# Performance work log

Hardware: AMD Instinct MI355X
Metric: run time of the kernel (lower is better)

## Reference

```python
import jax, jax.numpy as jnp
import numpy as np

NUM_NODES = 100000
NUM_EDGES = 600000
NUM_GRAPHS = 1000
EMB = 128


def setup_inputs() -> dict:
    key = jax.random.key(0)
    ks = jax.random.split(key, 12)
    x = jax.random.normal(ks[0], (NUM_NODES, 4), dtype=jnp.float32)
    edge_index = jax.random.randint(ks[1], (2, NUM_EDGES), 0, NUM_NODES, dtype=jnp.int32)
    x_scalar = jax.random.normal(ks[2], (NUM_GRAPHS, 4), dtype=jnp.float32)
    batch_index = jnp.sort(jax.random.randint(ks[3], (NUM_NODES,), 0, NUM_GRAPHS, dtype=jnp.int32))
    def glorot(k, shape):
        fan_in, fan_out = shape[0], shape[1]
        s = jnp.sqrt(2.0 / (fan_in + fan_out)).astype(jnp.float32)
        return jax.random.normal(k, shape, dtype=jnp.float32) * s
    return {
        "x": x,
        "edge_index": edge_index,
        "x_scalar": x_scalar,
        "batch_index": batch_index,
        "W0": glorot(ks[4], (4, EMB)), "b0": jnp.zeros((EMB,), jnp.float32),
        "W1": glorot(ks[5], (EMB, EMB)), "b1": jnp.zeros((EMB,), jnp.float32),
        "W2": glorot(ks[6], (EMB, EMB)), "b2": jnp.zeros((EMB,), jnp.float32),
        "W3": glorot(ks[7], (EMB, EMB)), "b3": jnp.zeros((EMB,), jnp.float32),
        "Wl1": glorot(ks[8], (EMB + 4, 64)), "bl1": jnp.zeros((64,), jnp.float32),
        "Wl2": glorot(ks[9], (64, 1)), "bl2": jnp.zeros((1,), jnp.float32),
    }


def _gcn_norm(edge_index, num_nodes):
    # PyG GCNConv default: add self-loops, symmetric normalization
    loop = jnp.arange(num_nodes, dtype=edge_index.dtype)
    src = jnp.concatenate([edge_index[0], loop])
    dst = jnp.concatenate([edge_index[1], loop])
    deg = jax.ops.segment_sum(jnp.ones_like(src, dtype=jnp.float32), dst,
                              num_segments=num_nodes)
    dinv = jnp.where(deg > 0, jax.lax.rsqrt(jnp.maximum(deg, 1e-12)), 0.0)
    norm = dinv[src] * dinv[dst]  # [E+N]
    return src, dst, norm


def _gcn_conv(h, src, dst, norm, W, b, num_nodes):
    h = h @ W                                   # [N, out]
    msg = h[src] * norm[:, None]                # gather + normalize
    out = jax.ops.segment_sum(msg, dst, num_segments=num_nodes)  # scatter-add
    return out + b


def reference(x, edge_index, x_scalar, batch_index,
              W0, b0, W1, b1, W2, b2, W3, b3, Wl1, bl1, Wl2, bl2):
    n = x.shape[0]
    src, dst, norm = _gcn_norm(edge_index, n)
    h = jax.nn.relu(_gcn_conv(x, src, dst, norm, W0, b0, n))
    h = jax.nn.relu(_gcn_conv(h, src, dst, norm, W1, b1, n))
    h = jax.nn.relu(_gcn_conv(h, src, dst, norm, W2, b2, n))
    h = jax.nn.relu(_gcn_conv(h, src, dst, norm, W3, b3, n))
    # global mean pool over batch_index
    sums = jax.ops.segment_sum(h, batch_index, num_segments=NUM_GRAPHS)
    cnts = jax.ops.segment_sum(jnp.ones((n,), jnp.float32), batch_index,
                               num_segments=NUM_GRAPHS)
    pooled = sums / jnp.maximum(cnts, 1.0)[:, None]          # [G, EMB]
    feat = jnp.concatenate([pooled, x_scalar], axis=1)       # [G, EMB+4]
    out = jax.nn.relu(feat @ Wl1 + bl1) @ Wl2 + bl2          # [G, 1]
    return out
```

## Files before the change

kernel.cpp:

```cpp
#include <hip/hip_runtime.h>

#define NN 100000
#define EE 600000
#define GG 1000
#define NB ((NN + 255) / 256)
#define CAP 32
#define LDSPAD 136

typedef __bf16 bf16x8 __attribute__((ext_vector_type(8)));
typedef float f32x4 __attribute__((ext_vector_type(4)));
typedef unsigned int u32;

__device__ inline float2 bf2_to_f2(u32 u) {
  return make_float2(__uint_as_float(u << 16), __uint_as_float(u & 0xffff0000u));
}
__device__ inline u32 f2_to_bf2(float a, float b) {
  union { __bf16 h[2]; u32 u; } pk;
  pk.h[0] = (__bf16)a; pk.h[1] = (__bf16)b;
  return pk.u;
}


__global__ void k_init(int* cnt, int* gstart) {
  int i = blockIdx.x * 256 + threadIdx.x;
  if (i < NN) cnt[i] = 0;
  if (i <= GG) gstart[i] = NN;
}

__global__ void k_fill(const int* __restrict__ src, const int* __restrict__ dst,
                       int* cnt, int* __restrict__ ibucket) {
  int e = blockIdx.x * 256 + threadIdx.x;
  if (e >= EE) return;
  int s = src[e], d = dst[e];
  int pos = atomicAdd(&cnt[d], 1);
  if (pos < CAP - 1) ibucket[d * CAP + pos] = s;
}

__global__ void k_prep(const int* __restrict__ cnt, float* __restrict__ dinv,
                       const int* __restrict__ batch, int* gstart,
                       const float* __restrict__ W1, const float* __restrict__ W2,
                       const float* __restrict__ W3,
                       __bf16* __restrict__ Wt1, __bf16* __restrict__ Wt2,
                       __bf16* __restrict__ Wt3) {
  int gid = blockIdx.x * 256 + threadIdx.x;
  if (gid < NN) {
    dinv[gid] = rsqrtf((float)(cnt[gid] + 1));
    int b = batch[gid];
    if (gid == 0) {
      for (int g = 0; g <= b; ++g) gstart[g] = 0;
    } else {
      int prev = batch[gid - 1];
      for (int g = prev + 1; g <= b; ++g) gstart[g] = gid;
    }
  }
  if (gid < 3 * 16384) {
    int which = gid >> 14, idx = gid & 16383;
    int n = idx >> 7, k = idx & 127;
    const float* W = (which == 0) ? W1 : (which == 1) ? W2 : W3;
    __bf16* Wt = (which == 0) ? Wt1 : (which == 1) ? Wt2 : Wt3;
    Wt[(size_t)n * 128 + k] = (__bf16)W[(size_t)k * 128 + n];
  }
}

__global__ void k_wb(const int* __restrict__ ibucket, const int* __restrict__ cnt,
                     const float* __restrict__ dinv, int2* __restrict__ wbucket) {
  int gid = blockIdx.x * 256 + threadIdx.x;
  if (gid >= NN * CAP) return;
  int d = gid >> 5, slot = gid & 31;
  int m = min(cnt[d], CAP - 1);
  int mp = (m + 8) & ~7;
  if (slot >= mp) return;
  float dd = dinv[d];
  int s; float w;
  if (slot < m)      { s = ibucket[gid]; w = dinv[s] * dd; }
  else if (slot == m){ s = d;            w = dd * dd; }
  else               { s = d;            w = 0.f; }
  wbucket[gid] = make_int2(s, __float_as_int(w));
}


__global__ void k_aggx(const float4* __restrict__ x, const int* __restrict__ cnt,
                       const int2* __restrict__ wbucket, float4* __restrict__ y) {
  int i = blockIdx.x * 256 + threadIdx.x;
  if (i >= NN) return;
  int m1 = min(cnt[i], CAP - 1) + 1;
  float4 acc = make_float4(0.f, 0.f, 0.f, 0.f);
  for (int e = 0; e < m1; ++e) {
    int2 md = wbucket[i * CAP + e];
    float w = __int_as_float(md.y);
    float4 v = x[md.x];
    acc.x = fmaf(w, v.x, acc.x);
    acc.y = fmaf(w, v.y, acc.y);
    acc.z = fmaf(w, v.z, acc.z);
    acc.w = fmaf(w, v.w, acc.w);
  }
  y[i] = acc;
}


__global__ void k_lin0(const float4* __restrict__ y, const float* __restrict__ W0,
                       const float* __restrict__ b0, u32* __restrict__ hout2) {
  int gid = blockIdx.x * 256 + threadIdx.x;
  if (gid >= NN * 16) return;
  int node = gid >> 4, cg = gid & 15;
  float4 yv = y[node];
  float v[8];
  #pragma unroll
  for (int k = 0; k < 2; ++k) {
    float4 b = *(const float4*)(b0 + cg * 8 + k * 4);
    v[k * 4 + 0] = b.x; v[k * 4 + 1] = b.y; v[k * 4 + 2] = b.z; v[k * 4 + 3] = b.w;
  }
  #pragma unroll
  for (int k = 0; k < 4; ++k) {
    float yk = (k == 0) ? yv.x : (k == 1) ? yv.y : (k == 2) ? yv.z : yv.w;
    float4 wa = *(const float4*)(W0 + k * 128 + cg * 8);
    float4 wb = *(const float4*)(W0 + k * 128 + cg * 8 + 4);
    v[0] = fmaf(yk, wa.x, v[0]); v[1] = fmaf(yk, wa.y, v[1]);
    v[2] = fmaf(yk, wa.z, v[2]); v[3] = fmaf(yk, wa.w, v[3]);
    v[4] = fmaf(yk, wb.x, v[4]); v[5] = fmaf(yk, wb.y, v[5]);
    v[6] = fmaf(yk, wb.z, v[6]); v[7] = fmaf(yk, wb.w, v[7]);
  }
  uint4 o;
  o.x = f2_to_bf2(fmaxf(v[0], 0.f), fmaxf(v[1], 0.f));
  o.y = f2_to_bf2(fmaxf(v[2], 0.f), fmaxf(v[3], 0.f));
  o.z = f2_to_bf2(fmaxf(v[4], 0.f), fmaxf(v[5], 0.f));
  o.w = f2_to_bf2(fmaxf(v[6], 0.f), fmaxf(v[7], 0.f));
  *(uint4*)(hout2 + (size_t)node * 64 + cg * 4) = o;
}

__global__ __launch_bounds__(256) void k_agg23(const __bf16* __restrict__ hlin,
                                               const int* __restrict__ cnt,
                                               const int2* __restrict__ wbucket,
                                               u32* __restrict__ hout2) {
  int node = blockIdx.x * 4 + (threadIdx.x >> 6);
  int lane = threadIdx.x & 63;
  int ln = lane & 15, quad = lane >> 4;
  if (node >= NN) return;
  int mp = (min(cnt[node], CAP - 1) + 8) & ~7;
  int2 me = wbucket[(size_t)node * CAP + (lane & 31)];
  int s_l = me.x, w_l = me.y;

  float acc[8] = {0.f, 0.f, 0.f, 0.f, 0.f, 0.f, 0.f, 0.f};
  for (int j = 0; j < mp; j += 8) {
    int p0 = (j + quad) * 4, p1 = (j + 4 + quad) * 4;
    int se0 = __builtin_amdgcn_ds_bpermute(p0, s_l);
    int se1 = __builtin_amdgcn_ds_bpermute(p1, s_l);
    float w0e = __int_as_float(__builtin_amdgcn_ds_bpermute(p0, w_l));
    float w1e = __int_as_float(__builtin_amdgcn_ds_bpermute(p1, w_l));
    uint4 u0 = *(const uint4*)(hlin + ((size_t)se0 << 7) + ln * 8);
    uint4 u1 = *(const uint4*)(hlin + ((size_t)se1 << 7) + ln * 8);
    float2 f;
    f = bf2_to_f2(u0.x); acc[0] = fmaf(w0e, f.x, acc[0]); acc[1] = fmaf(w0e, f.y, acc[1]);
    f = bf2_to_f2(u0.y); acc[2] = fmaf(w0e, f.x, acc[2]); acc[3] = fmaf(w0e, f.y, acc[3]);
    f = bf2_to_f2(u0.z); acc[4] = fmaf(w0e, f.x, acc[4]); acc[5] = fmaf(w0e, f.y, acc[5]);
    f = bf2_to_f2(u0.w); acc[6] = fmaf(w0e, f.x, acc[6]); acc[7] = fmaf(w0e, f.y, acc[7]);
    f = bf2_to_f2(u1.x); acc[0] = fmaf(w1e, f.x, acc[0]); acc[1] = fmaf(w1e, f.y, acc[1]);
    f = bf2_to_f2(u1.y); acc[2] = fmaf(w1e, f.x, acc[2]); acc[3] = fmaf(w1e, f.y, acc[3]);
    f = bf2_to_f2(u1.z); acc[4] = fmaf(w1e, f.x, acc[4]); acc[5] = fmaf(w1e, f.y, acc[5]);
    f = bf2_to_f2(u1.w); acc[6] = fmaf(w1e, f.x, acc[6]); acc[7] = fmaf(w1e, f.y, acc[7]);
  }
  #pragma unroll
  for (int k = 0; k < 8; ++k) {
    acc[k] += __shfl_xor(acc[k], 16);
    acc[k] += __shfl_xor(acc[k], 32);
  }
  if (quad == 0) {
    uint4 o;
    o.x = f2_to_bf2(acc[0], acc[1]);
    o.y = f2_to_bf2(acc[2], acc[3]);
    o.z = f2_to_bf2(acc[4], acc[5]);
    o.w = f2_to_bf2(acc[6], acc[7]);
    *(uint4*)(hout2 + (size_t)node * 64 + ln * 4) = o;
  }
}

__global__ __launch_bounds__(256) void k_mfma(const __bf16* __restrict__ hin,
                                              const __bf16* __restrict__ Wt,
                                              const float* __restrict__ bias,
                                              __bf16* __restrict__ hout) {
  __shared__ __bf16 As[128 * LDSPAD];
  int tid = threadIdx.x;
  int row0 = blockIdx.x * 128;
  int lane = tid & 63, w = tid >> 6;
  int ln = lane & 15, quad = lane >> 4;

  bf16x8 bfrag[8][4];
  float bcol[8];
  #pragma unroll
  for (int nt = 0; nt < 8; ++nt) {
    bcol[nt] = bias[nt * 16 + ln];
    #pragma unroll
    for (int kc = 0; kc < 4; ++kc)
      bfrag[nt][kc] = *(const bf16x8*)(Wt + (size_t)(nt * 16 + ln) * 128 + kc * 32 + quad * 8);
  }

  #pragma unroll
  for (int i = 0; i < 8; ++i) {
    int eb = (i * 256 + tid) * 8;
    int r = eb >> 7, c = eb & 127;
    int gr = row0 + r;
    uint4 v = make_uint4(0, 0, 0, 0);
    if (gr < NN) v = *(const uint4*)(hin + (size_t)gr * 128 + c);
    *(uint4*)&As[r * LDSPAD + c] = v;
  }
  __syncthreads();

  f32x4 acc[2][8];
  #pragma unroll
  for (int rt = 0; rt < 2; ++rt)
    #pragma unroll
    for (int nt = 0; nt < 8; ++nt) acc[rt][nt] = (f32x4){0.f, 0.f, 0.f, 0.f};

  #pragma unroll
  for (int kc = 0; kc < 4; ++kc) {
    bf16x8 a0 = *(const bf16x8*)&As[(w * 32 + ln) * LDSPAD + kc * 32 + quad * 8];
    bf16x8 a1 = *(const bf16x8*)&As[(w * 32 + 16 + ln) * LDSPAD + kc * 32 + quad * 8];
    #pragma unroll
    for (int nt = 0; nt < 8; ++nt) {
      acc[0][nt] = __builtin_amdgcn_mfma_f32_16x16x32_bf16(a0, bfrag[nt][kc], acc[0][nt], 0, 0, 0);
      acc[1][nt] = __builtin_amdgcn_mfma_f32_16x16x32_bf16(a1, bfrag[nt][kc], acc[1][nt], 0, 0, 0);
    }
  }

  #pragma unroll
  for (int rt = 0; rt < 2; ++rt)
    #pragma unroll
    for (int nt = 0; nt < 8; ++nt)
      #pragma unroll
      for (int reg = 0; reg < 4; ++reg) {
        int gr = row0 + w * 32 + rt * 16 + quad * 4 + reg;
        if (gr < NN)
          hout[(size_t)gr * 128 + nt * 16 + ln] =
              (__bf16)fmaxf(acc[rt][nt][reg] + bcol[nt], 0.f);
      }
}

__global__ __launch_bounds__(256) void k_poolmlp(const uint2* __restrict__ h4u,
                                                 const int* __restrict__ gstart,
                                                 const float* __restrict__ xs,
                                                 const float* __restrict__ Wl1,
                                                 const float* __restrict__ bl1,
                                                 const float* __restrict__ Wl2,
                                                 const float* __restrict__ bl2,
                                                 float* __restrict__ out) {
  __shared__ float4 part[8][32];
  __shared__ float pooled[128];
  int g = blockIdx.x;
  int beg = gstart[g], end = gstart[g + 1];
  int tid = threadIdx.x;
  int cg = tid & 31;
  int rg = tid >> 5;
  float4 acc = make_float4(0.f, 0.f, 0.f, 0.f);
  for (int i = beg + rg; i < end; i += 8) {
    uint2 u = h4u[(size_t)i * 32 + cg];
    acc.x += __uint_as_float(u.x << 16);
    acc.y += __uint_as_float(u.x & 0xffff0000u);
    acc.z += __uint_as_float(u.y << 16);
    acc.w += __uint_as_float(u.y & 0xffff0000u);
  }
  part[rg][cg] = acc;
  __syncthreads();
  if (tid < 32) {
    float4 s = part[0][tid];
    #pragma unroll
    for (int r = 1; r < 8; ++r) {
      float4 v = part[r][tid];
      s.x += v.x; s.y += v.y; s.z += v.z; s.w += v.w;
    }
    float sc = 1.f / fmaxf((float)(end - beg), 1.f);
    pooled[tid * 4 + 0] = s.x * sc;
    pooled[tid * 4 + 1] = s.y * sc;
    pooled[tid * 4 + 2] = s.z * sc;
    pooled[tid * 4 + 3] = s.w * sc;
  }
  __syncthreads();
  if (tid < 64) {
    float hj = bl1[tid];
    #pragma unroll 4
    for (int k = 0; k < 128; ++k) hj = fmaf(pooled[k], Wl1[k * 64 + tid], hj);
    const float* xr = xs + g * 4;
    #pragma unroll
    for (int k = 0; k < 4; ++k) hj = fmaf(xr[k], Wl1[(128 + k) * 64 + tid], hj);
    hj = fmaxf(hj, 0.f);
    float val = hj * Wl2[tid];
    #pragma unroll
    for (int off = 32; off > 0; off >>= 1) val += __shfl_down(val, off);
    if (tid == 0) out[g] = val + bl2[0];
  }
}


extern "C" void kernel_launch(void* const* d_in, const int* in_sizes, int n_in,
                              void* d_out, int out_size, void* d_ws, size_t ws_size,
                              hipStream_t stream) {
  const float* x    = (const float*)d_in[0];
  const int*   ei   = (const int*)d_in[1];
  const float* xs   = (const float*)d_in[2];
  const int*   batch= (const int*)d_in[3];
  const float* W0   = (const float*)d_in[4];
  const float* b0   = (const float*)d_in[5];
  const float* W1   = (const float*)d_in[6];
  const float* b1   = (const float*)d_in[7];
  const float* W2   = (const float*)d_in[8];
  const float* b2   = (const float*)d_in[9];
  const float* W3   = (const float*)d_in[10];
  const float* b3   = (const float*)d_in[11];
  const float* Wl1  = (const float*)d_in[12];
  const float* bl1  = (const float*)d_in[13];
  const float* Wl2  = (const float*)d_in[14];
  const float* bl2  = (const float*)d_in[15];
  const int* srcA = ei;
  const int* dstA = ei + EE;
  float* out = (float*)d_out;

  char* p = (char*)d_ws;
  auto take = [&](size_t bytes) { char* q = p; p += (bytes + 255) & ~(size_t)255; return q; };
  __bf16* hA    = (__bf16*)take((size_t)NN * 128 * 2);
  __bf16* hB    = (__bf16*)take((size_t)NN * 128 * 2);
  float*  y     = (float*)take((size_t)NN * 4 * 4);
  int*    cnt   = (int*)take((size_t)NN * 4);
  float*  dinv  = (float*)take((size_t)NN * 4);
  int*    ibucket = (int*)take((size_t)NN * CAP * 4);
  int2*   wbucket = (int2*)take((size_t)NN * CAP * 8);
  int*    gstart= (int*)take((size_t)(GG + 1) * 4);
  __bf16* Wt1   = (__bf16*)take(16384 * 2);
  __bf16* Wt2   = (__bf16*)take(16384 * 2);
  __bf16* Wt3   = (__bf16*)take(16384 * 2);

  k_init<<<NB, 256, 0, stream>>>(cnt, gstart);
  k_fill<<<(EE + 255) / 256, 256, 0, stream>>>(srcA, dstA, cnt, ibucket);
  k_prep<<<NB, 256, 0, stream>>>(cnt, dinv, batch, gstart, W1, W2, W3, Wt1, Wt2, Wt3);
  k_wb<<<(NN * CAP + 255) / 256, 256, 0, stream>>>(ibucket, cnt, dinv, wbucket);

  k_aggx<<<NB, 256, 0, stream>>>((const float4*)x, cnt, wbucket, (float4*)y);
  k_lin0<<<(NN * 16 + 255) / 256, 256, 0, stream>>>((const float4*)y, W0, b0, (u32*)hA);
  k_agg23<<<(NN + 3) / 4, 256, 0, stream>>>(hA, cnt, wbucket, (u32*)hB);
  k_mfma<<<(NN + 127) / 128, 256, 0, stream>>>(hB, Wt1, b1, hA);
  k_agg23<<<(NN + 3) / 4, 256, 0, stream>>>(hA, cnt, wbucket, (u32*)hB);
  k_mfma<<<(NN + 127) / 128, 256, 0, stream>>>(hB, Wt2, b2, hA);
  k_agg23<<<(NN + 3) / 4, 256, 0, stream>>>(hA, cnt, wbucket, (u32*)hB);
  k_mfma<<<(NN + 127) / 128, 256, 0, stream>>>(hB, Wt3, b3, hA);

  k_poolmlp<<<GG, 256, 0, stream>>>((const uint2*)hA, gstart, xs, Wl1, bl1, Wl2, bl2, out);
}
```

Before: 354.9 us.

## Fuse degree-norm and weighted-bucket prep; use wave-per-node first-layer aggregation

The separate dinv prep and weight-bucket kernels are merged into one launch that recomputes rsqrt of degree counts inline, so the dinv array and one kernel launch go away. The first-layer 4-wide aggregation now assigns one wavefront per node, with lanes split across neighbor slots and feature components, permute broadcasts of the bucket entries, and a shuffle reduction. This replaces a serial per-thread loop that had load imbalance. The merged kernel now writes all 32 slots per node instead of only the padded count, which adds memory writes.

```diff
diff --git a/kernel.cpp b/kernel.cpp
--- a/kernel.cpp
+++ b/kernel.cpp
@@ -36,15 +36,26 @@
   if (pos < CAP - 1) ibucket[d * CAP + pos] = s;
 }
 
-__global__ void k_prep(const int* __restrict__ cnt, float* __restrict__ dinv,
-                       const int* __restrict__ batch, int* gstart,
-                       const float* __restrict__ W1, const float* __restrict__ W2,
-                       const float* __restrict__ W3,
-                       __bf16* __restrict__ Wt1, __bf16* __restrict__ Wt2,
-                       __bf16* __restrict__ Wt3) {
+__global__ void k_prep2(const int* __restrict__ ibucket, const int* __restrict__ cnt,
+                        int2* __restrict__ wbucket,
+                        const int* __restrict__ batch, int* gstart,
+                        const float* __restrict__ W1, const float* __restrict__ W2,
+                        const float* __restrict__ W3,
+                        __bf16* __restrict__ Wt1, __bf16* __restrict__ Wt2,
+                        __bf16* __restrict__ Wt3) {
   int gid = blockIdx.x * 256 + threadIdx.x;
+  if (gid < NN * CAP) {
+    int d = gid >> 5, slot = gid & 31;
+    int cd = cnt[d];
+    int m = min(cd, CAP - 1);
+    float dd = rsqrtf((float)(cd + 1));
+    int s; float w;
+    if (slot < m)       { s = ibucket[gid]; w = rsqrtf((float)(cnt[s] + 1)) * dd; }
+    else if (slot == m) { s = d;            w = dd * dd; }
+    else                { s = d;            w = 0.f; }
+    wbucket[gid] = make_int2(s, __float_as_int(w));
+  }
   if (gid < NN) {
-    dinv[gid] = rsqrtf((float)(cnt[gid] + 1));
     int b = batch[gid];
     if (gid == 0) {
       for (int g = 0; g <= b; ++g) gstart[g] = 0;
@@ -62,39 +73,32 @@
   }
 }
 
-__global__ void k_wb(const int* __restrict__ ibucket, const int* __restrict__ cnt,
-                     const float* __restrict__ dinv, int2* __restrict__ wbucket) {
-  int gid = blockIdx.x * 256 + threadIdx.x;
-  if (gid >= NN * CAP) return;
-  int d = gid >> 5, slot = gid & 31;
-  int m = min(cnt[d], CAP - 1);
-  int mp = (m + 8) & ~7;
-  if (slot >= mp) return;
-  float dd = dinv[d];
-  int s; float w;
-  if (slot < m)      { s = ibucket[gid]; w = dinv[s] * dd; }
-  else if (slot == m){ s = d;            w = dd * dd; }
-  else               { s = d;            w = 0.f; }
-  wbucket[gid] = make_int2(s, __float_as_int(w));
-}
-
-
-__global__ void k_aggx(const float4* __restrict__ x, const int* __restrict__ cnt,
-                       const int2* __restrict__ wbucket, float4* __restrict__ y) {
-  int i = blockIdx.x * 256 + threadIdx.x;
-  if (i >= NN) return;
-  int m1 = min(cnt[i], CAP - 1) + 1;
-  float4 acc = make_float4(0.f, 0.f, 0.f, 0.f);
-  for (int e = 0; e < m1; ++e) {
-    int2 md = wbucket[i * CAP + e];
-    float w = __int_as_float(md.y);
-    float4 v = x[md.x];
-    acc.x = fmaf(w, v.x, acc.x);
-    acc.y = fmaf(w, v.y, acc.y);
-    acc.z = fmaf(w, v.z, acc.z);
-    acc.w = fmaf(w, v.w, acc.w);
-  }
-  y[i] = acc;
+__global__ __launch_bounds__(256) void k_aggx(const float* __restrict__ x,
+                                              const int* __restrict__ cnt,
+                                              const int2* __restrict__ wbucket,
+                                              float* __restrict__ y) {
+  int node = blockIdx.x * 4 + (threadIdx.x >> 6);
+  int lane = threadIdx.x & 63;
+  if (node >= NN) return;
+  int slot = lane & 15, d = lane >> 4;
+  int2 me = wbucket[(size_t)node * CAP + (lane & 31)];
+  int mp = (min(cnt[node], CAP - 1) + 8) & ~7;
+
+  int p = slot * 4;
+  int s0 = __builtin_amdgcn_ds_bpermute(p, me.x);
+  float w0 = __int_as_float(__builtin_amdgcn_ds_bpermute(p, me.y));
+  float acc = w0 * x[(size_t)s0 * 4 + d];
+  if (mp > 16) {
+    int p2 = (16 + slot) * 4;
+    int s1 = __builtin_amdgcn_ds_bpermute(p2, me.x);
+    float w1 = __int_as_float(__builtin_amdgcn_ds_bpermute(p2, me.y));
+    acc = fmaf(w1, x[(size_t)s1 * 4 + d], acc);
+  }
+  acc += __shfl_xor(acc, 1);
+  acc += __shfl_xor(acc, 2);
+  acc += __shfl_xor(acc, 4);
+  acc += __shfl_xor(acc, 8);
+  if (slot == 0) y[(size_t)node * 4 + d] = acc;
 }
 
 
@@ -319,7 +323,6 @@
   __bf16* hB    = (__bf16*)take((size_t)NN * 128 * 2);
   float*  y     = (float*)take((size_t)NN * 4 * 4);
   int*    cnt   = (int*)take((size_t)NN * 4);
-  float*  dinv  = (float*)take((size_t)NN * 4);
   int*    ibucket = (int*)take((size_t)NN * CAP * 4);
   int2*   wbucket = (int2*)take((size_t)NN * CAP * 8);
   int*    gstart= (int*)take((size_t)(GG + 1) * 4);
@@ -329,10 +332,11 @@
 
   k_init<<<NB, 256, 0, stream>>>(cnt, gstart);
   k_fill<<<(EE + 255) / 256, 256, 0, stream>>>(srcA, dstA, cnt, ibucket);
-  k_prep<<<NB, 256, 0, stream>>>(cnt, dinv, batch, gstart, W1, W2, W3, Wt1, Wt2, Wt3);
-  k_wb<<<(NN * CAP + 255) / 256, 256, 0, stream>>>(ibucket, cnt, dinv, wbucket);
-
-  k_aggx<<<NB, 256, 0, stream>>>((const float4*)x, cnt, wbucket, (float4*)y);
+  k_prep2<<<(NN * CAP + 255) / 256, 256, 0, stream>>>(ibucket, cnt, wbucket,
+                                                      batch, gstart, W1, W2, W3,
+                                                      Wt1, Wt2, Wt3);
+
+  k_aggx<<<(NN + 3) / 4, 256, 0, stream>>>(x, cnt, wbucket, y);
   k_lin0<<<(NN * 16 + 255) / 256, 256, 0, stream>>>((const float4*)y, W0, b0, (u32*)hA);
   k_agg23<<<(NN + 3) / 4, 256, 0, stream>>>(hA, cnt, wbucket, (u32*)hB);
   k_mfma<<<(NN + 127) / 128, 256, 0, stream>>>(hB, Wt1, b1, hA);
```

Result: no change. 356.0 us (+0.3%).
